# Kernel tuning notes

Hardware: AMD Instinct MI355X
Metric: run time of the kernel (lower is better)

## Reference

```python
import jax, jax.numpy as jnp
import numpy as np

EMBED_DIM = 1024
NUM_HEAD = 16
HEAD_DIM = EMBED_DIM // NUM_HEAD
SCALE = HEAD_DIM ** -0.5


def setup_inputs() -> dict:
    key = jax.random.key(0)
    ks = jax.random.split(key, 8)
    B, N, K, D = 2, 2048, 2048, EMBED_DIM
    s = D ** -0.5
    return {
        "x": jax.random.normal(ks[0], (B, N, D), jnp.float32),
        "ctx": jax.random.normal(ks[1], (B, K, D), jnp.float32),
        "Wq": jax.random.normal(ks[2], (D, D), jnp.float32) * s,
        "bq": jnp.zeros((D,), jnp.float32),
        "Wkv": jax.random.normal(ks[3], (D, 2 * D), jnp.float32) * s,
        "bkv": jnp.zeros((2 * D,), jnp.float32),
        "Wproj": jax.random.normal(ks[4], (D, D), jnp.float32) * s,
        "bproj": jnp.zeros((D,), jnp.float32),
    }


def reference(x, ctx, Wq, bq, Wkv, bkv, Wproj, bproj):
    B, N, D = x.shape
    K = ctx.shape[1]
    H, hd = NUM_HEAD, HEAD_DIM
    # Q projection -> [B, H, N, hd]
    q = (x @ Wq + bq).reshape(B, N, H, hd).transpose(0, 2, 1, 3)
    # KV projection -> k, v each [B, H, K, hd]
    kv = (ctx @ Wkv + bkv).reshape(B, K, 2, H, hd).transpose(2, 0, 3, 1, 4)
    k, v = kv[0], kv[1]
    # scaled dot-product attention with materialized scores [B, H, N, K]
    attn = jnp.einsum("bhnd,bhkd->bhnk", q * SCALE, k)
    attn = jax.nn.softmax(attn, axis=-1)
    out = jnp.einsum("bhnk,bhkd->bhnd", attn, v)
    out = out.transpose(0, 2, 1, 3).reshape(B, N, D)
    return out @ Wproj + bproj
```

## Files before the change

kernel.cpp:

```cpp
#include <hip/hip_runtime.h>
#include <hip/hip_bf16.h>

typedef __attribute__((ext_vector_type(8))) short bf16x8;
typedef __attribute__((ext_vector_type(4))) float f32x4;
typedef __attribute__((ext_vector_type(16))) float f32x16;
typedef unsigned short u16;
typedef unsigned int u32;

#define NUM_HEAD 16
#define HEAD_DIM 64
#define SEQ_N 2048
#define SEQ_K 2048
#define EMB 1024
#define MROWS 4096
static constexpr float ATTN_SCALE_LOG2E = 0.125f * 1.44269504f;

#if __has_builtin(__builtin_amdgcn_exp2f)
#define EXP2(x) __builtin_amdgcn_exp2f(x)
#else
#define EXP2(x) __expf(0.69314718056f * (x))
#endif

__device__ __forceinline__ u16 f2bf(float f) {
  __hip_bfloat16 h = __float2bfloat16(f);
  return *reinterpret_cast<u16*>(&h);
}

__device__ __forceinline__ u32 pack2(float lo, float hi) {
  __hip_bfloat162 h = __float22bfloat162_rn(make_float2(lo, hi));
  return *reinterpret_cast<u32*>(&h);
}

__device__ __forceinline__ void plswap(u32& a, u32& b) {
  auto r = __builtin_amdgcn_permlane32_swap(a, b, false, false);
  a = r[0]; b = r[1];
}

__device__ __forceinline__ void async16(const u16* g, u16* l) {
  __builtin_amdgcn_global_load_lds(
      (const __attribute__((address_space(1))) unsigned int*)g,
      (__attribute__((address_space(3))) unsigned int*)l, 16, 0, 0);
}

__global__ __launch_bounds__(256) void cvt2(const float* __restrict__ x,
                                            const float* __restrict__ ctx,
                                            u16* __restrict__ xb, u16* __restrict__ cb) {
  const int n4 = MROWS * EMB / 4;
  int gid = blockIdx.x * 256 + threadIdx.x;
  const float4* s; ushort4* d; int i;
  if (gid < n4) { s = (const float4*)x;   d = (ushort4*)xb; i = gid; }
  else          { s = (const float4*)ctx; d = (ushort4*)cb; i = gid - n4; }
  float4 v = s[i];
  ushort4 o;
  o.x = f2bf(v.x); o.y = f2bf(v.y); o.z = f2bf(v.z); o.w = f2bf(v.w);
  d[i] = o;
}

__global__ __launch_bounds__(256) void transpose_cvt4(
    const float* __restrict__ Wq, const float* __restrict__ Wkv,
    const float* __restrict__ Wproj,
    u16* __restrict__ Wqt, u16* __restrict__ Wkvt, u16* __restrict__ Wpt) {
  __shared__ float tile[32][33];
  const int z = blockIdx.z;
  const float* W; u16* Wt; int srcN, colbase;
  if (z == 0)      { W = Wq;    Wt = Wqt;                          srcN = 1024; colbase = 0; }
  else if (z == 1) { W = Wkv;   Wt = Wkvt;                         srcN = 2048; colbase = 0; }
  else if (z == 2) { W = Wkv;   Wt = Wkvt + (size_t)1024 * 1024;   srcN = 2048; colbase = 1024; }
  else             { W = Wproj; Wt = Wpt;                          srcN = 1024; colbase = 0; }
  int n0 = blockIdx.x * 32, k0 = blockIdx.y * 32;
  int tx = threadIdx.x & 31, ty = threadIdx.x >> 5;
  #pragma unroll
  for (int i = ty; i < 32; i += 8)
    tile[i][tx] = W[(size_t)(k0 + i) * srcN + colbase + n0 + tx];
  __syncthreads();
  #pragma unroll
  for (int i = ty; i < 32; i += 8)
    Wt[(size_t)(n0 + i) * 1024 + k0 + tx] = f2bf(tile[tx][i]);
}

__global__ __launch_bounds__(256, 3) void gemm_qkv(
    const u16* __restrict__ xb, const u16* __restrict__ cb,
    const u16* __restrict__ Wqt, const u16* __restrict__ Wkvt,
    const float* __restrict__ bq, const float* __restrict__ bkv,
    u16* __restrict__ Qb, u16* __restrict__ Kb, u16* __restrict__ Vtb)
{
  __shared__ alignas(16) u16 smem[(64 + 256) * 64];
  u16* As = smem;
  u16* Bs = smem + 64 * 64;
  const int tid = threadIdx.x;
  const bool isQ = (blockIdx.y < 4);
  const int n0 = (isQ ? blockIdx.y : blockIdx.y - 4) * 256;
  const int m0 = blockIdx.x * 64;
  const u16* A      = isQ ? xb : cb;
  const u16* Wt     = isQ ? Wqt : Wkvt;
  const float* bias = isQ ? bq : bkv;
  const int wave = tid >> 6, lane = tid & 63;
  const int wm = (wave >> 1) * 32, wn = (wave & 1) * 128;
  const int l15 = lane & 15, quad = lane >> 4;

  f32x4 acc[2][8];
  #pragma unroll
  for (int i = 0; i < 2; i++)
    #pragma unroll
    for (int j = 0; j < 8; j++)
      #pragma unroll
      for (int r = 0; r < 4; r++) acc[i][j][r] = 0.0f;

  const int srow = tid >> 3;
  const int scol = (tid & 7) * 8;
  const u16* ag = A + (size_t)(m0 + srow) * EMB + scol;
  const u16* bg = Wt + (size_t)(n0 + srow) * EMB + scol;
  const int ldsoff = tid * 8;

  for (int kt = 0; kt < EMB; kt += 64) {
    #pragma unroll
    for (int s = 0; s < 2; s++)
      async16(ag + (size_t)(s * 32) * EMB + kt, &As[ldsoff + s * 2048]);
    #pragma unroll
    for (int s = 0; s < 8; s++)
      async16(bg + (size_t)(s * 32) * EMB + kt, &Bs[ldsoff + s * 2048]);
    __syncthreads();
    #pragma unroll
    for (int ks = 0; ks < 2; ks++) {
      bf16x8 af[2], bfr[8];
      #pragma unroll
      for (int i = 0; i < 2; i++)
        af[i]  = *(const bf16x8*)&As[(wm + i * 16 + l15) * 64 + ks * 32 + quad * 8];
      #pragma unroll
      for (int j = 0; j < 8; j++)
        bfr[j] = *(const bf16x8*)&Bs[(wn + j * 16 + l15) * 64 + ks * 32 + quad * 8];
      #pragma unroll
      for (int i = 0; i < 2; i++)
        #pragma unroll
        for (int j = 0; j < 8; j++)
          acc[i][j] = __builtin_amdgcn_mfma_f32_16x16x32_bf16(af[i], bfr[j], acc[i][j], 0, 0, 0);
    }
    __syncthreads();
  }

  if (isQ) {
    #pragma unroll
    for (int i = 0; i < 2; i++) {
      #pragma unroll
      for (int j = 0; j < 8; j++) {
        const int gc = n0 + wn + j * 16 + l15;
        const float bv = bias[gc];
        const int h = gc >> 6, d = gc & 63;
        #pragma unroll
        for (int r = 0; r < 4; r++) {
          const int gm = m0 + wm + i * 16 + quad * 4 + r;
          const int bb = gm >> 11, nn = gm & 2047;
          Qb[((size_t)(bb * NUM_HEAD + h) * SEQ_N + nn) * HEAD_DIM + d] =
              f2bf((acc[i][j][r] + bv) * ATTN_SCALE_LOG2E);
        }
      }
    }
  } else {
    const int s = n0 >> 10;
    if (s == 0) {
      #pragma unroll
      for (int i = 0; i < 2; i++) {
        #pragma unroll
        for (int j = 0; j < 8; j++) {
          const int gc = n0 + wn + j * 16 + l15;
          const float bv = bias[gc];
          const int h = gc >> 6, d = gc & 63;
          #pragma unroll
          for (int r = 0; r < 4; r++) {
            const int gm = m0 + wm + i * 16 + quad * 4 + r;
            const int bb = gm >> 11, kk = gm & 2047;
            Kb[((size_t)(bb * NUM_HEAD + h) * SEQ_K + kk) * HEAD_DIM + d] =
                f2bf(acc[i][j][r] + bv);
          }
        }
      }
    } else {
      u16* wbuf = smem + wave * 1280;
      const int gm0 = m0 + wm;
      const int bb = gm0 >> 11;
      const int kk0 = gm0 & 2047;
      const int hbase = ((n0 + wn) >> 6) & 15;
      #pragma unroll
      for (int hh2 = 0; hh2 < 2; hh2++) {
        #pragma unroll
        for (int p = 0; p < 2; p++) {
          #pragma unroll
          for (int jj = 0; jj < 2; jj++) {
            const int j = hh2 * 4 + p * 2 + jj;
            const int gc = n0 + wn + j * 16 + l15;
            const float bv = bias[gc];
            #pragma unroll
            for (int i = 0; i < 2; i++) {
              ushort4 pk;
              pk.x = f2bf(acc[i][j][0] + bv);
              pk.y = f2bf(acc[i][j][1] + bv);
              pk.z = f2bf(acc[i][j][2] + bv);
              pk.w = f2bf(acc[i][j][3] + bv);
              *(ushort4*)&wbuf[(jj * 16 + l15) * 40 + i * 16 + quad * 4] = pk;
            }
          }
          __syncthreads();
          u32* dstu = (u32*)(Vtb +
              ((size_t)(bb * NUM_HEAD + hbase + hh2) * HEAD_DIM + p * 32) * SEQ_K + kk0);
          #pragma unroll
          for (int it = 0; it < 8; it++) {
            const int dd = it * 4 + quad;
            const int kp = l15 * 2;
            u32 v = *(const u32*)&wbuf[dd * 40 + kp];
            dstu[(size_t)dd * (SEQ_K / 2) + (kp >> 1)] = v;
          }
          __syncthreads();
        }
      }
    }
  }
}

__global__ __launch_bounds__(256) void gemm_proj(
    const u16* __restrict__ A, const u16* __restrict__ Wt,
    const float* __restrict__ bias, float* __restrict__ outF)
{
  __shared__ alignas(16) u16 smem[(64 + 128) * 64];
  u16* As = smem;
  u16* Bs = smem + 64 * 64;
  const int tid = threadIdx.x;
  const int n0 = blockIdx.y * 128, m0 = blockIdx.x * 64;
  const int wave = tid >> 6, lane = tid & 63;
  const int wm = (wave >> 1) * 32, wn = (wave & 1) * 64;
  const int l15 = lane & 15, quad = lane >> 4;

  f32x4 acc[2][4];
  #pragma unroll
  for (int i = 0; i < 2; i++)
    #pragma unroll
    for (int j = 0; j < 4; j++)
      #pragma unroll
      for (int r = 0; r < 4; r++) acc[i][j][r] = 0.0f;

  const int srow = tid >> 3;
  const int scol = (tid & 7) * 8;
  const u16* ag = A + (size_t)(m0 + srow) * EMB + scol;
  const u16* bg = Wt + (size_t)(n0 + srow) * EMB + scol;
  const int ldsoff = tid * 8;

  for (int kt = 0; kt < EMB; kt += 64) {
    async16(ag + kt, &As[ldsoff]);
    async16(ag + (size_t)32 * EMB + kt, &As[ldsoff + 2048]);
    #pragma unroll
    for (int s = 0; s < 4; s++)
      async16(bg + (size_t)(s * 32) * EMB + kt, &Bs[ldsoff + s * 2048]);
    __syncthreads();
    #pragma unroll
    for (int ks = 0; ks < 2; ks++) {
      bf16x8 af[2], bfr[4];
      #pragma unroll
      for (int i = 0; i < 2; i++)
        af[i]  = *(const bf16x8*)&As[(wm + i * 16 + l15) * 64 + ks * 32 + quad * 8];
      #pragma unroll
      for (int j = 0; j < 4; j++)
        bfr[j] = *(const bf16x8*)&Bs[(wn + j * 16 + l15) * 64 + ks * 32 + quad * 8];
      #pragma unroll
      for (int i = 0; i < 2; i++)
        #pragma unroll
        for (int j = 0; j < 4; j++)
          acc[i][j] = __builtin_amdgcn_mfma_f32_16x16x32_bf16(af[i], bfr[j], acc[i][j], 0, 0, 0);
    }
    __syncthreads();
  }

  #pragma unroll
  for (int i = 0; i < 2; i++) {
    #pragma unroll
    for (int j = 0; j < 4; j++) {
      const int gc = n0 + wn + j * 16 + l15;
      const float bv = bias[gc];
      #pragma unroll
      for (int r = 0; r < 4; r++) {
        const int gm = m0 + wm + i * 16 + quad * 4 + r;
        outF[(size_t)gm * EMB + gc] = acc[i][j][r] + bv;
      }
    }
  }
}

__global__ __launch_bounds__(512) void attn_kernel(
    const u16* __restrict__ Qb, const u16* __restrict__ Kb,
    const u16* __restrict__ Vtb, u16* __restrict__ Ob)
{
  __shared__ alignas(16) u16 Ks[2][64 * 64];
  __shared__ alignas(16) u16 Vs[2][64 * 64];
  const int tid = threadIdx.x;
  const int bh = blockIdx.x;
  const int m0 = blockIdx.y * 256;
  const int wave = tid >> 6, lane = tid & 63;
  const int l31 = lane & 31, hi = lane >> 5;
  const int hi16 = hi * 16;
  const int swz = (lane & 7) << 4;
  const int rowb = m0 + wave * 32;

  bf16x8 bq[4];
  {
    const u16* qp = Qb + ((size_t)bh * SEQ_N + rowb + l31) * HEAD_DIM + hi * 8;
    #pragma unroll
    for (int db = 0; db < 4; db++) bq[db] = *(const bf16x8*)(qp + db * 16);
  }

  f32x16 o0, o1;
  #pragma unroll
  for (int r = 0; r < 16; r++) { o0[r] = 0.f; o1[r] = 0.f; }
  float l_part = 0.f;

  const int srow = tid >> 3;
  const int sg   = (tid & 7) ^ (srow & 7);
  const u16* kg = Kb  + (size_t)bh * SEQ_K * HEAD_DIM;
  const u16* vg = Vtb + (size_t)bh * HEAD_DIM * SEQ_K;
  const int ldst = tid * 8;

#define STAGE(kt_, nb_) do {                                              \
    async16(kg + (size_t)((kt_) + srow) * HEAD_DIM + sg * 8, &Ks[nb_][ldst]); \
    async16(vg + (size_t)srow * SEQ_K + (kt_) + sg * 8, &Vs[nb_][ldst]);      \
  } while (0)

  STAGE(0, 0);
  __syncthreads();

  for (int kt = 0; kt < SEQ_K; kt += 64) {
    const int cur = (kt >> 6) & 1;
    if (kt + 64 < SEQ_K) STAGE(kt + 64, cur ^ 1);
    const char* KsB = (const char*)Ks[cur];
    const char* VsB = (const char*)Vs[cur];

    #pragma unroll
    for (int g = 0; g < 2; g++) {
      f32x16 s;
      #pragma unroll
      for (int r = 0; r < 16; r++) s[r] = 0.f;
      #pragma unroll
      for (int db = 0; db < 4; db++) {
        const bf16x8 ka = *(const bf16x8*)(
            KsB + (g * 32 + l31) * 128 + ((db * 32 + hi16) ^ swz));
        s = __builtin_amdgcn_mfma_f32_32x32x16_bf16(ka, bq[db], s, 0, 0, 0);
      }

      float p[16];
      #pragma unroll
      for (int r = 0; r < 16; r++) p[r] = EXP2(s[r]);
      #pragma unroll
      for (int r = 0; r < 16; r++) l_part += p[r];
      u32 w0 = pack2(p[0],  p[1]),  w1 = pack2(p[2],  p[3]);
      u32 w2 = pack2(p[4],  p[5]),  w3 = pack2(p[6],  p[7]);
      u32 w4 = pack2(p[8],  p[9]),  w5 = pack2(p[10], p[11]);
      u32 w6 = pack2(p[12], p[13]), w7 = pack2(p[14], p[15]);
      plswap(w0, w2); plswap(w1, w3);
      plswap(w4, w6); plswap(w5, w7);
      union PU { u32 u[4]; bf16x8 v; } pa0, pa1;
      pa0.u[0] = w0; pa0.u[1] = w1; pa0.u[2] = w2; pa0.u[3] = w3;
      pa1.u[0] = w4; pa1.u[1] = w5; pa1.u[2] = w6; pa1.u[3] = w7;

      bf16x8 vb;
      vb = *(const bf16x8*)(VsB + (l31)*128      + ((g * 64 + hi16)      ^ swz));
      o0 = __builtin_amdgcn_mfma_f32_32x32x16_bf16(pa0.v, vb, o0, 0, 0, 0);
      vb = *(const bf16x8*)(VsB + (l31)*128      + ((g * 64 + 32 + hi16) ^ swz));
      o0 = __builtin_amdgcn_mfma_f32_32x32x16_bf16(pa1.v, vb, o0, 0, 0, 0);
      vb = *(const bf16x8*)(VsB + (32 + l31)*128 + ((g * 64 + hi16)      ^ swz));
      o1 = __builtin_amdgcn_mfma_f32_32x32x16_bf16(pa0.v, vb, o1, 0, 0, 0);
      vb = *(const bf16x8*)(VsB + (32 + l31)*128 + ((g * 64 + 32 + hi16) ^ swz));
      o1 = __builtin_amdgcn_mfma_f32_32x32x16_bf16(pa1.v, vb, o1, 0, 0, 0);
    }
    __syncthreads();
  }
#undef STAGE

  const float lsum = l_part + __shfl_xor(l_part, 32, 64);
  const float inv = 1.0f / lsum;

  const int bb = bh >> 4, hh = bh & 15;
  #pragma unroll
  for (int r = 0; r < 16; r++) {
    const int qrow = (r & 3) + 8 * (r >> 2) + 4 * hi;
    const float invr = __shfl(inv, qrow, 64);
    const int gm = rowb + qrow;
    u16* op = Ob + ((size_t)bb * SEQ_N + gm) * EMB + hh * HEAD_DIM + l31;
    op[0]  = f2bf(o0[r] * invr);
    op[32] = f2bf(o1[r] * invr);
  }
}

extern "C" void kernel_launch(void* const* d_in, const int* in_sizes, int n_in,
                              void* d_out, int out_size, void* d_ws, size_t ws_size,
                              hipStream_t stream)
{
  const float* x     = (const float*)d_in[0];
  const float* ctx   = (const float*)d_in[1];
  const float* Wq    = (const float*)d_in[2];
  const float* bq    = (const float*)d_in[3];
  const float* Wkv   = (const float*)d_in[4];
  const float* bkv   = (const float*)d_in[5];
  const float* Wproj = (const float*)d_in[6];
  const float* bproj = (const float*)d_in[7];
  float* out = (float*)d_out;

  char* ws = (char*)d_ws;
  size_t off = 0;
  auto walloc = [&](size_t bytes) -> void* {
    void* p = ws + off;
    off += (bytes + 255) & ~(size_t)255;
    return p;
  };
  u16* xb   = (u16*)walloc((size_t)MROWS * EMB * 2);
  u16* cb   = (u16*)walloc((size_t)MROWS * EMB * 2);
  u16* Wqt  = (u16*)walloc((size_t)EMB * EMB * 2);
  u16* Wkvt = (u16*)walloc((size_t)2 * EMB * EMB * 2);
  u16* Wpt  = (u16*)walloc((size_t)EMB * EMB * 2);
  u16* Qb   = (u16*)walloc((size_t)MROWS * EMB * 2);
  u16* Kb   = (u16*)walloc((size_t)MROWS * EMB * 2);
  u16* Vtb  = (u16*)walloc((size_t)MROWS * EMB * 2);
  u16* Ob   = (u16*)walloc((size_t)MROWS * EMB * 2);

  cvt2<<<8192, 256, 0, stream>>>(x, ctx, xb, cb);
  transpose_cvt4<<<dim3(32, 32, 4), 256, 0, stream>>>(Wq, Wkv, Wproj, Wqt, Wkvt, Wpt);
  gemm_qkv<<<dim3(64, 12), 256, 0, stream>>>(xb, cb, Wqt, Wkvt, bq, bkv, Qb, Kb, Vtb);
  attn_kernel<<<dim3(32, 8), 512, 0, stream>>>(Qb, Kb, Vtb, Ob);
  gemm_proj<<<dim3(64, 8), 256, 0, stream>>>(Ob, Wpt, bproj, out);
}
```

Baseline: 215.1 us.

## Restructure attention kernel: 128-key tiles, 4-wave blocks, batched QK MFMAs, setprio

The attention kernel now uses 256-thread blocks of 4 waves, each covering 128 query rows, and a grid of 32x16 instead of 32x8. K and V are staged in 128-key tiles with a wider XOR swizzle for the 128-wide V rows. All four QK^T score tiles are computed together before the softmax and PV stage, the row sums use tree reductions, and s_setprio raises priority around the MFMA sections. The aim is fewer barriers per key, more independent MFMA work to hide latency, and two blocks per CU. The cost is doubled LDS per block and more registers held for the four score accumulators.

```diff
diff --git a/kernel.cpp b/kernel.cpp
--- a/kernel.cpp
+++ b/kernel.cpp
@@ -283,19 +283,20 @@
   }
 }
 
-__global__ __launch_bounds__(512) void attn_kernel(
+__global__ __launch_bounds__(256, 2) void attn_kernel(
     const u16* __restrict__ Qb, const u16* __restrict__ Kb,
     const u16* __restrict__ Vtb, u16* __restrict__ Ob)
 {
-  __shared__ alignas(16) u16 Ks[2][64 * 64];
-  __shared__ alignas(16) u16 Vs[2][64 * 64];
+  __shared__ alignas(16) u16 Ks[2][128 * 64];
+  __shared__ alignas(16) u16 Vs[2][64 * 128];
   const int tid = threadIdx.x;
   const int bh = blockIdx.x;
-  const int m0 = blockIdx.y * 256;
+  const int m0 = blockIdx.y * 128;
   const int wave = tid >> 6, lane = tid & 63;
   const int l31 = lane & 31, hi = lane >> 5;
   const int hi16 = hi * 16;
-  const int swz = (lane & 7) << 4;
+  const int swzK = (l31 & 7) << 4;
+  const int swzV = (l31 & 15) << 4;
   const int rowb = m0 + wave * 32;
 
   bf16x8 bq[4];
@@ -308,45 +309,58 @@
   f32x16 o0, o1;
   #pragma unroll
   for (int r = 0; r < 16; r++) { o0[r] = 0.f; o1[r] = 0.f; }
-  float l_part = 0.f;
-
-  const int srow = tid >> 3;
-  const int sg   = (tid & 7) ^ (srow & 7);
+  float l4[4] = {0.f, 0.f, 0.f, 0.f};
+
+  const int krow0 = tid >> 3;
+  const int ksg   = (tid & 7) ^ (krow0 & 7);
+  const int vrow0 = tid >> 4;
+  const int vsg   = (tid & 15) ^ vrow0;
   const u16* kg = Kb  + (size_t)bh * SEQ_K * HEAD_DIM;
   const u16* vg = Vtb + (size_t)bh * HEAD_DIM * SEQ_K;
-  const int ldst = tid * 8;
-
-#define STAGE(kt_, nb_) do {                                              \
-    async16(kg + (size_t)((kt_) + srow) * HEAD_DIM + sg * 8, &Ks[nb_][ldst]); \
-    async16(vg + (size_t)srow * SEQ_K + (kt_) + sg * 8, &Vs[nb_][ldst]);      \
+
+#define STAGE(kt_, nb_) do {                                                   \
+    _Pragma("unroll")                                                          \
+    for (int s = 0; s < 4; s++) {                                              \
+      async16(kg + (size_t)((kt_) + s * 32 + krow0) * HEAD_DIM + ksg * 8,      \
+              &Ks[nb_][s * 2048 + tid * 8]);                                   \
+      async16(vg + (size_t)(s * 16 + vrow0) * SEQ_K + (kt_) + vsg * 8,         \
+              &Vs[nb_][s * 2048 + tid * 8]);                                   \
+    }                                                                          \
   } while (0)
 
   STAGE(0, 0);
   __syncthreads();
 
-  for (int kt = 0; kt < SEQ_K; kt += 64) {
-    const int cur = (kt >> 6) & 1;
-    if (kt + 64 < SEQ_K) STAGE(kt + 64, cur ^ 1);
+  for (int kt = 0; kt < SEQ_K; kt += 128) {
+    const int cur = (kt >> 7) & 1;
+    if (kt + 128 < SEQ_K) STAGE(kt + 128, cur ^ 1);
     const char* KsB = (const char*)Ks[cur];
     const char* VsB = (const char*)Vs[cur];
 
-    #pragma unroll
-    for (int g = 0; g < 2; g++) {
-      f32x16 s;
-      #pragma unroll
-      for (int r = 0; r < 16; r++) s[r] = 0.f;
-      #pragma unroll
-      for (int db = 0; db < 4; db++) {
+    f32x16 sg[4];
+    #pragma unroll
+    for (int g = 0; g < 4; g++)
+      #pragma unroll
+      for (int r = 0; r < 16; r++) sg[g][r] = 0.f;
+    __builtin_amdgcn_s_setprio(1);
+    #pragma unroll
+    for (int db = 0; db < 4; db++) {
+      #pragma unroll
+      for (int g = 0; g < 4; g++) {
         const bf16x8 ka = *(const bf16x8*)(
-            KsB + (g * 32 + l31) * 128 + ((db * 32 + hi16) ^ swz));
-        s = __builtin_amdgcn_mfma_f32_32x32x16_bf16(ka, bq[db], s, 0, 0, 0);
+            KsB + (g * 32 + l31) * 128 + ((db * 32 + hi16) ^ swzK));
+        sg[g] = __builtin_amdgcn_mfma_f32_32x32x16_bf16(ka, bq[db], sg[g], 0, 0, 0);
       }
-
+    }
+    __builtin_amdgcn_s_setprio(0);
+
+    #pragma unroll
+    for (int g = 0; g < 4; g++) {
       float p[16];
       #pragma unroll
-      for (int r = 0; r < 16; r++) p[r] = EXP2(s[r]);
-      #pragma unroll
-      for (int r = 0; r < 16; r++) l_part += p[r];
+      for (int r = 0; r < 16; r++) p[r] = EXP2(sg[g][r]);
+      l4[g] += (((p[0] + p[1]) + (p[2] + p[3])) + ((p[4] + p[5]) + (p[6] + p[7])))
+             + (((p[8] + p[9]) + (p[10] + p[11])) + ((p[12] + p[13]) + (p[14] + p[15])));
       u32 w0 = pack2(p[0],  p[1]),  w1 = pack2(p[2],  p[3]);
       u32 w2 = pack2(p[4],  p[5]),  w3 = pack2(p[6],  p[7]);
       u32 w4 = pack2(p[8],  p[9]),  w5 = pack2(p[10], p[11]);
@@ -358,19 +372,22 @@
       pa1.u[0] = w4; pa1.u[1] = w5; pa1.u[2] = w6; pa1.u[3] = w7;
 
       bf16x8 vb;
-      vb = *(const bf16x8*)(VsB + (l31)*128      + ((g * 64 + hi16)      ^ swz));
+      __builtin_amdgcn_s_setprio(1);
+      vb = *(const bf16x8*)(VsB + (l31)*256      + ((g * 64 + hi16)      ^ swzV));
       o0 = __builtin_amdgcn_mfma_f32_32x32x16_bf16(pa0.v, vb, o0, 0, 0, 0);
-      vb = *(const bf16x8*)(VsB + (l31)*128      + ((g * 64 + 32 + hi16) ^ swz));
+      vb = *(const bf16x8*)(VsB + (l31)*256      + ((g * 64 + 32 + hi16) ^ swzV));
       o0 = __builtin_amdgcn_mfma_f32_32x32x16_bf16(pa1.v, vb, o0, 0, 0, 0);
-      vb = *(const bf16x8*)(VsB + (32 + l31)*128 + ((g * 64 + hi16)      ^ swz));
+      vb = *(const bf16x8*)(VsB + (32 + l31)*256 + ((g * 64 + hi16)      ^ swzV));
       o1 = __builtin_amdgcn_mfma_f32_32x32x16_bf16(pa0.v, vb, o1, 0, 0, 0);
-      vb = *(const bf16x8*)(VsB + (32 + l31)*128 + ((g * 64 + 32 + hi16) ^ swz));
+      vb = *(const bf16x8*)(VsB + (32 + l31)*256 + ((g * 64 + 32 + hi16) ^ swzV));
       o1 = __builtin_amdgcn_mfma_f32_32x32x16_bf16(pa1.v, vb, o1, 0, 0, 0);
+      __builtin_amdgcn_s_setprio(0);
     }
     __syncthreads();
   }
 #undef STAGE
 
+  const float l_part = (l4[0] + l4[1]) + (l4[2] + l4[3]);
   const float lsum = l_part + __shfl_xor(l_part, 32, 64);
   const float inv = 1.0f / lsum;
 
@@ -420,6 +437,6 @@
   cvt2<<<8192, 256, 0, stream>>>(x, ctx, xb, cb);
   transpose_cvt4<<<dim3(32, 32, 4), 256, 0, stream>>>(Wq, Wkv, Wproj, Wqt, Wkvt, Wpt);
   gemm_qkv<<<dim3(64, 12), 256, 0, stream>>>(xb, cb, Wqt, Wkvt, bq, bkv, Qb, Kb, Vtb);
-  attn_kernel<<<dim3(32, 8), 512, 0, stream>>>(Qb, Kb, Vtb, Ob);
+  attn_kernel<<<dim3(32, 16), 256, 0, stream>>>(Qb, Kb, Vtb, Ob);
   gemm_proj<<<dim3(64, 8), 256, 0, stream>>>(Ob, Wpt, bproj, out);
 }
```

New measurement: 211.2 us. About the same (-1.8%).
